# Kernel tuning notes

Hardware: AMD Instinct MI355X
Metric: run time of the kernel (lower is better)

Reference implementation:

```python
import jax, jax.numpy as jnp
import numpy as np

# SLAYER neuron / simulation constants (from params)
THETA = 10.0      # spike threshold
TAU_SR = 10.0     # PSP (synaptic response) time constant
TS = 1.0          # simulation time step
TAU_RHO = 1.0     # surrogate-gradient width
SCALE_RHO = 1.0   # surrogate-gradient scale
ALPHA = float(np.exp(-TS / TAU_SR))  # leaky-filter decay per step

B, C_IN, T = 32, 156, 2048
HID, OUT = 512, 20


@jax.custom_vjp
def spike(u):
    # Hard threshold with SLAYER-style exponential surrogate gradient.
    return (u >= THETA).astype(u.dtype)

def _spike_fwd(u):
    return spike(u), u

def _spike_bwd(u, g):
    sg = (SCALE_RHO / TAU_RHO) * jnp.exp(-jnp.abs(u - THETA) / TAU_RHO)
    return (g * sg,)

spike.defvjp(_spike_fwd, _spike_bwd)


def psp(x):
    # Leaky exponential temporal filter along the LAST axis (SLAYER psp):
    # y[t] = ALPHA * y[t-1] + x[t]
    xt = jnp.moveaxis(x, -1, 0)  # [T, ...]
    def step(c, xi):
        c = ALPHA * c + xi
        return c, c
    _, y = jax.lax.scan(step, jnp.zeros_like(xt[0]), xt)
    return jnp.moveaxis(y, 0, -1)


def dense(x, W):
    # SLAYER dense layer: per-timestep fully-connected over channel dim.
    # x: [N, C, H, W, T], W: [O, C] -> [N, O, H, W, T]
    return jnp.einsum('oc,nchwt->nohwt', W, x)


def _make_perm():
    rng = np.random.default_rng(0)
    random_list = rng.permutation(np.arange(1, 40))
    perm = []
    for i in random_list:
        perm.append(2 * int(i) - 2)
        perm.append(2 * int(i) - 1)
    for i in random_list:
        perm.append(2 * int(i) - 2 + 78)
        perm.append(2 * int(i) - 1 + 78)
    return jnp.asarray(perm, dtype=jnp.int32)


def setup_inputs() -> dict:
    key = jax.random.key(0)
    k0, k1, k2, k3, k4 = jax.random.split(key, 5)
    spike_input = jax.random.randint(k0, (B, C_IN, 1, 1, T), 0, 2).astype(jnp.float32)
    W1 = jax.random.normal(k1, (HID, C_IN), dtype=jnp.float32) * (C_IN ** -0.5)
    W2 = jax.random.normal(k2, (OUT, HID), dtype=jnp.float32) * (HID ** -0.5)
    Wl1 = jax.random.normal(k3, (HID, T), dtype=jnp.float32) * (T ** -0.5)
    Wl2 = jax.random.normal(k4, (OUT, HID), dtype=jnp.float32) * (HID ** -0.5)
    perm = _make_perm()
    return {"spike_input": spike_input, "W1": W1, "W2": W2,
            "Wl1": Wl1, "Wl2": Wl2, "perm": perm}


def reference(spike_input, W1, W2, Wl1, Wl2, perm):
    # Branch 1: channel-dense over taxels, PSP + spike, twice.
    s1 = spike(psp(dense(spike_input, W1)))          # [B, HID, 1, 1, T]
    spike_output = spike(psp(dense(s1, W2)))         # [B, OUT, 1, 1, T]

    # Branch 2: transpose channel<->time, permute taxel axis, dense over time dim.
    x_t = jnp.swapaxes(spike_input, 1, 4)            # [B, T, 1, 1, C_IN]
    x_tp = x_t[..., perm]                            # gather on taxel axis
    l1 = spike(psp(dense(x_tp, Wl1)))                # [B, HID, 1, 1, C_IN]
    location_output = spike(psp(dense(l1, Wl2)))     # [B, OUT, 1, 1, C_IN]

    return jnp.concatenate([spike_output, location_output], axis=4)
```

## Files before the change

### kernel.cpp

```cpp
#include <hip/hip_runtime.h>

#define ALPHA  0.90483741803595952f
#define ALPHA8 0.44932896411722156f
#define THETA  10.0f
#define BF1    ((unsigned short)0x3F80)
#define ISCALE 0.015625f

typedef short   bf16x8 __attribute__((ext_vector_type(8)));
typedef float   f32x4  __attribute__((ext_vector_type(4)));
typedef float   f32x4v __attribute__((ext_vector_type(4)));
typedef unsigned short ushort4v __attribute__((ext_vector_type(4)));
typedef unsigned short ushort8v __attribute__((ext_vector_type(8)));
typedef unsigned char  uchar4v  __attribute__((ext_vector_type(4)));
typedef unsigned char  uchar8v  __attribute__((ext_vector_type(8)));
typedef long long i64;

__device__ __forceinline__ unsigned short f2bf(float f) {
    unsigned int x = __float_as_uint(f);
    unsigned int r = (x + 0x7FFFu + ((x >> 16) & 1u)) >> 16;
    return (unsigned short)r;
}
__device__ __forceinline__ float bf2f(unsigned short h) {
    return __uint_as_float(((unsigned int)h) << 16);
}
__device__ __forceinline__ void split2(float w, unsigned short& h0,
                                       unsigned short& h1) {
    h0 = f2bf(w);          float r0 = w - bf2f(h0);
    h1 = f2bf(r0);
}
__device__ __forceinline__ unsigned char f2fp8(float f) {
    int pk = __builtin_amdgcn_cvt_pk_fp8_f32(f, 0.f, 0, false);
    return (unsigned char)(pk & 0xFF);
}
__device__ __forceinline__ float fp82f(unsigned char b) {
    return __builtin_amdgcn_cvt_f32_fp8((int)b, 0);
}

__global__ __launch_bounds__(256) void prep_scan_pack(
    const float* __restrict__ In, unsigned char* __restrict__ Infp8,
    unsigned short* __restrict__ Pbf,
    const float* __restrict__ W1,  const float* __restrict__ W2,
    const float* __restrict__ Wl1, const float* __restrict__ Wl2,
    unsigned short* __restrict__ W1p,  unsigned char* __restrict__ W2p8,
    unsigned char* __restrict__ Wl1p8, unsigned short* __restrict__ Wl2p)
{
    const int blk = blockIdx.x;
    if (blk >= 4992) {
        const int bidx = blk - 4992;
        if (bidx >= 512 && bidx < 544) {
            int m = bidx - 512;
            for (int k = threadIdx.x; k < 512; k += 256) {
                float w = (m < 20) ? W2[(long long)m * 512 + k] : 0.f;
                unsigned char h0 = f2fp8(w);
                unsigned char h1 = f2fp8(w - fp82f(h0));
                W2p8[(long long)m * 512 + k] = h0;
                W2p8[16384 + (long long)m * 512 + k] = h1;
            }
        } else if (bidx >= 544 && bidx < 1056) {
            int m = bidx - 544;
            for (int k = threadIdx.x; k < 2048; k += 256) {
                float w = Wl1[(long long)m * 2048 + k] * 64.0f;
                unsigned char h0 = f2fp8(w);
                unsigned char h1 = f2fp8(w - fp82f(h0));
                Wl1p8[(long long)m * 2048 + k] = h0;
                Wl1p8[1048576 + (long long)m * 2048 + k] = h1;
            }
        } else {
            const float* W; unsigned short* P; int M, K, Kp, Mp, m;
            if (bidx < 512) { W = W1;  P = W1p;  M = 512; K = 156; Kp = 160; Mp = 512; m = bidx; }
            else            { W = Wl2; P = Wl2p; M = 20;  K = 512; Kp = 512; Mp = 32;  m = bidx - 1056; }
            for (int k = threadIdx.x; k < Kp; k += 256) {
                float v = (m < M && k < K) ? W[(long long)m * K + k] : 0.f;
                unsigned short h0, h1;
                split2(v, h0, h1);
                P[(long long)m * Kp + k] = h0;
                P[(long long)Mp * Kp + (long long)m * Kp + k] = h1;
            }
        }
        return;
    }

    const int row = blk;
    const int tid = threadIdx.x;
    const float* x = In + (long long)row * 2048 + tid * 8;
    const unsigned char ONE8 = f2fp8(1.0f);

    float v[8];
    *(f32x4v*)&v[0] = *(const f32x4v*)x;
    *(f32x4v*)&v[4] = *(const f32x4v*)(x + 4);

    uchar8v raw;
    #pragma unroll
    for (int k = 0; k < 8; ++k) raw[k] = (v[k] >= 0.5f) ? ONE8 : (unsigned char)0;
    *(uchar8v*)(Infp8 + (long long)row * 2048 + tid * 8) = raw;

    float y = 0.f;
    #pragma unroll
    for (int k = 0; k < 8; ++k) { y = ALPHA * y + v[k]; v[k] = y; }

    __shared__ float sc[256];
    float val = y;
    sc[tid] = val;
    float m = ALPHA8;
    for (int d = 1; d < 256; d <<= 1) {
        __syncthreads();
        float p = (tid >= d) ? sc[tid - d] : 0.f;
        __syncthreads();
        val += m * p;
        sc[tid] = val;
        m *= m;
    }
    __syncthreads();
    float carry = (tid > 0) ? sc[tid - 1] : 0.f;

    ushort8v pv;
    float ak = ALPHA;
    #pragma unroll
    for (int k = 0; k < 8; ++k) {
        float yk = v[k] + ak * carry;
        ak *= ALPHA;
        pv[k] = f2bf(yk);
    }
    *(ushort8v*)(Pbf + (long long)row * 2048 + tid * 8) = pv;
}

__global__ __launch_bounds__(256) void transposeP(
    const unsigned short* __restrict__ Pbf, unsigned short* __restrict__ PT)
{
    __shared__ unsigned short Tile[64][72];
    const int t0 = blockIdx.x * 64;
    const int c0 = blockIdx.y * 64;
    const int b  = blockIdx.z;
    const int tid = threadIdx.x;

    #pragma unroll
    for (int s = 0; s < 2; ++s) {
        int id = tid + s * 256;
        int cc = id >> 3;
        int t8 = (id & 7) * 8;
        ushort8v v = {0,0,0,0,0,0,0,0};
        if (c0 + cc < 156)
            v = *(const ushort8v*)(Pbf + (long long)(b * 156 + c0 + cc) * 2048 + t0 + t8);
        *(ushort8v*)&Tile[cc][t8] = v;
    }
    __syncthreads();

    #pragma unroll
    for (int s = 0; s < 2; ++s) {
        int id = tid + s * 256;
        int t  = id >> 3;
        int c8 = (id & 7) * 8;
        if (c0 + c8 + 7 < 160) {
            unsigned short r[8];
            #pragma unroll
            for (int j = 0; j < 8; ++j) r[j] = Tile[c8 + j][t];
            *(ushort8v*)(PT + (long long)b * 327680 + (long long)(t0 + t) * 160 + c0 + c8)
                = *(ushort8v*)r;
        }
    }
}

__global__ __launch_bounds__(256) void mega_gemm1(
    const unsigned short* __restrict__ W1p,
    const unsigned short* __restrict__ PT,
    unsigned short* __restrict__ S1bits,
    const unsigned char* __restrict__ Wl1p8,
    const unsigned char* __restrict__ Infp8,
    unsigned short* __restrict__ Zp)
{
    __shared__ alignas(16) unsigned char SMEM[30720];
    const int bx  = blockIdx.x;
    const int tid = threadIdx.x;
    const int lane = tid & 63, w = tid >> 6;
    const int wy = w >> 1, wx = w & 1;
    const int l15 = lane & 15, kq = lane >> 4;

    if (bx < 2048) {
        auto As = (unsigned short (*)[128][40])SMEM;
        auto Bs = (unsigned short (*)[40])(SMEM + 20480);

        const int z  = bx >> 6;
        const int m0 = ((bx >> 4) & 3) * 128;
        const int n0 = (bx & 15) * 128;
        const unsigned short* Tb = PT + (long long)z * 327680;

        int aPl[4], aM[4], aK8[4];
        #pragma unroll
        for (int s = 0; s < 4; ++s) {
            int id = tid + s * 256;
            aPl[s] = id >> 9; int rem = id & 511;
            aM[s] = rem >> 2; aK8[s] = (rem & 3) * 8;
        }
        int bT[2], bC8[2];
        #pragma unroll
        for (int s = 0; s < 2; ++s) {
            int id = tid + s * 256;
            bT[s] = id >> 2; bC8[s] = (id & 3) * 8;
        }

        f32x4 acc[4][4] = {};
        ushort8v aReg[4], bReg[2];

        #pragma unroll
        for (int s = 0; s < 4; ++s)
            aReg[s] = *(const ushort8v*)(W1p + (long long)aPl[s] * 81920 +
                                         (long long)(m0 + aM[s]) * 160 + aK8[s]);
        #pragma unroll
        for (int s = 0; s < 2; ++s)
            bReg[s] = *(const ushort8v*)(Tb + (long long)(n0 + bT[s]) * 160 + bC8[s]);
        #pragma unroll
        for (int s = 0; s < 4; ++s) *(ushort8v*)&As[aPl[s]][aM[s]][aK8[s]] = aReg[s];
        #pragma unroll
        for (int s = 0; s < 2; ++s) *(ushort8v*)&Bs[bT[s]][bC8[s]] = bReg[s];
        __syncthreads();

        #pragma unroll
        for (int it = 0; it < 5; ++it) {
            const int kn = (it + 1) * 32;
            if (it < 4) {
                #pragma unroll
                for (int s = 0; s < 4; ++s)
                    aReg[s] = *(const ushort8v*)(W1p + (long long)aPl[s] * 81920 +
                                                 (long long)(m0 + aM[s]) * 160 + kn + aK8[s]);
                #pragma unroll
                for (int s = 0; s < 2; ++s)
                    bReg[s] = *(const ushort8v*)(Tb + (long long)(n0 + bT[s]) * 160 + kn + bC8[s]);
            }

            bf16x8 bfr[4];
            #pragma unroll
            for (int nt = 0; nt < 4; ++nt)
                bfr[nt] = *(const bf16x8*)&Bs[wx * 64 + nt * 16 + l15][kq * 8];
            #pragma unroll
            for (int s = 0; s < 2; ++s) {
                #pragma unroll
                for (int mt = 0; mt < 4; ++mt) {
                    bf16x8 afr = *(const bf16x8*)&As[s][wy * 64 + mt * 16 + l15][kq * 8];
                    #pragma unroll
                    for (int nt = 0; nt < 4; ++nt)
                        acc[mt][nt] = __builtin_amdgcn_mfma_f32_16x16x32_bf16(
                            afr, bfr[nt], acc[mt][nt], 0, 0, 0);
                }
            }
            __syncthreads();
            if (it < 4) {
                #pragma unroll
                for (int s = 0; s < 4; ++s) *(ushort8v*)&As[aPl[s]][aM[s]][aK8[s]] = aReg[s];
                #pragma unroll
                for (int s = 0; s < 2; ++s) *(ushort8v*)&Bs[bT[s]][bC8[s]] = bReg[s];
                __syncthreads();
            }
        }

        unsigned short* Db = S1bits + (long long)z * 512 * 128;
        #pragma unroll
        for (int mt = 0; mt < 4; ++mt) {
            #pragma unroll
            for (int i = 0; i < 4; ++i) {
                int m = m0 + wy * 64 + mt * 16 + kq * 4 + i;
                #pragma unroll
                for (int nt = 0; nt < 4; ++nt) {
                    unsigned long long mask = __ballot(acc[mt][nt][i] >= THETA);
                    if (l15 == 0) {
                        int nchunk = (n0 + wx * 64 + nt * 16) >> 4;
                        Db[(long long)m * 128 + nchunk] =
                            (unsigned short)((mask >> (kq * 16)) & 0xFFFFu);
                    }
                }
            }
        }
    } else {
        auto As8 = (unsigned char (*)[64][72])SMEM;
        auto Bs8 = (unsigned char (*)[72])(SMEM + 9216);

        const int id0 = bx - 2048;
        const int nIdx = id0 % 40;
        if (nIdx >= 39) return;
        const int rest = id0 / 40;
        const int n0  = nIdx * 128;
        const int m0  = (rest & 7) * 64;
        const int ksl = rest >> 3;
        const int ks0 = ksl * 512;

        int aPl[4], aM[4], aK8[4];
        #pragma unroll
        for (int s = 0; s < 4; ++s) {
            int id = tid + s * 256;
            aPl[s] = id >> 9; int rem = id & 511;
            aM[s] = rem >> 3; aK8[s] = (rem & 7) * 8;
        }
        int bN[4], bK8[4];
        #pragma unroll
        for (int s = 0; s < 4; ++s) {
            int id = tid + s * 256;
            bN[s] = id >> 3; bK8[s] = (id & 7) * 8;
        }

        f32x4 acc[2][4] = {};
        uchar8v aReg[4], bReg[4];

        #pragma unroll
        for (int s = 0; s < 4; ++s)
            aReg[s] = *(const uchar8v*)(Wl1p8 + (long long)aPl[s] * 1048576 +
                                        (long long)(m0 + aM[s]) * 2048 + ks0 + aK8[s]);
        #pragma unroll
        for (int s = 0; s < 4; ++s)
            bReg[s] = *(const uchar8v*)(Infp8 + (long long)(n0 + bN[s]) * 2048 + ks0 + bK8[s]);
        #pragma unroll
        for (int s = 0; s < 4; ++s) *(uchar8v*)&As8[aPl[s]][aM[s]][aK8[s]] = aReg[s];
        #pragma unroll
        for (int s = 0; s < 4; ++s) *(uchar8v*)&Bs8[bN[s]][bK8[s]] = bReg[s];
        __syncthreads();

        for (int it = 0; it < 8; ++it) {
            const int kn = ks0 + (it + 1) * 64;
            if (it < 7) {
                #pragma unroll
                for (int s = 0; s < 4; ++s)
                    aReg[s] = *(const uchar8v*)(Wl1p8 + (long long)aPl[s] * 1048576 +
                                                (long long)(m0 + aM[s]) * 2048 + kn + aK8[s]);
                #pragma unroll
                for (int s = 0; s < 4; ++s)
                    bReg[s] = *(const uchar8v*)(Infp8 + (long long)(n0 + bN[s]) * 2048 + kn + bK8[s]);
            }

            #pragma unroll
            for (int ks = 0; ks < 2; ++ks) {
                i64 bfr[4];
                #pragma unroll
                for (int nt = 0; nt < 4; ++nt)
                    bfr[nt] = *(const i64*)&Bs8[wx * 64 + nt * 16 + l15][ks * 32 + kq * 8];
                #pragma unroll
                for (int s = 0; s < 2; ++s) {
                    #pragma unroll
                    for (int mt = 0; mt < 2; ++mt) {
                        i64 afr = *(const i64*)&As8[s][wy * 32 + mt * 16 + l15][ks * 32 + kq * 8];
                        #pragma unroll
                        for (int nt = 0; nt < 4; ++nt)
                            acc[mt][nt] = __builtin_amdgcn_mfma_f32_16x16x32_fp8_fp8(
                                afr, bfr[nt], acc[mt][nt], 0, 0, 0);
                    }
                }
            }
            __syncthreads();
            if (it < 7) {
                #pragma unroll
                for (int s = 0; s < 4; ++s) *(uchar8v*)&As8[aPl[s]][aM[s]][aK8[s]] = aReg[s];
                #pragma unroll
                for (int s = 0; s < 4; ++s) *(uchar8v*)&Bs8[bN[s]][bK8[s]] = bReg[s];
                __syncthreads();
            }
        }

        unsigned short* Tu = (unsigned short*)SMEM;
        #pragma unroll
        for (int mt = 0; mt < 2; ++mt) {
            #pragma unroll
            for (int i = 0; i < 4; ++i) {
                int mL = wy * 32 + mt * 16 + kq * 4 + i;
                #pragma unroll
                for (int nt = 0; nt < 4; ++nt) {
                    int nL = wx * 64 + nt * 16 + l15;
                    Tu[mL * 129 + nL] = f2bf(acc[mt][nt][i] * ISCALE);
                }
            }
        }
        __syncthreads();

        unsigned short* Zs = Zp + (long long)ksl * 2555904;
        #pragma unroll
        for (int s2 = 0; s2 < 32; ++s2) {
            int id = tid + s2 * 256;
            int cL = id >> 6;
            int mL = id & 63;
            int n = n0 + cL;
            int bb = n / 156, cc = n - bb * 156;
            Zs[(long long)cc * 16384 + bb * 512 + m0 + mL] = Tu[mL * 129 + cL];
        }
    }
}

__global__ __launch_bounds__(256) void mega_stage2(
    const unsigned char* __restrict__ W2p8,
    const unsigned short* __restrict__ S1bits,
    float* __restrict__ C2p,
    const unsigned short* __restrict__ Zp,
    const int* __restrict__ perm,
    unsigned short* __restrict__ L1T)
{
    __shared__ alignas(16) unsigned char SMEM[20608];
    const int bx  = blockIdx.x;
    const int tid = threadIdx.x;

    if (bx < 1024) {
        auto As = (unsigned char (*)[32][72])SMEM;
        auto Bs = (unsigned char (*)[72])(SMEM + 4608);

        const int lane = tid & 63, w = tid >> 6;
        const int l15 = lane & 15, kq = lane >> 4;
        const int n0  = (bx & 15) * 128;
        const int ksl = (bx >> 4) & 1;
        const int b   = bx >> 5;
        const int ks0 = ksl * 256;

        const unsigned short* Bb = S1bits + (long long)b * 512 * 128;
        const unsigned char ONE8 = f2fp8(1.0f);

        int aPl[2], aM[2], aK8[2];
        #pragma unroll
        for (int s = 0; s < 2; ++s) {
            int id = tid + s * 256;
            aPl[s] = id >> 8; int rem = id & 255;
            aM[s] = rem >> 3; aK8[s] = (rem & 7) * 8;
        }
        const int kb = (tid >> 4) * 4;
        const int nb = (tid & 15) * 8;
        const int nchunk = (n0 + nb) >> 4;
        const int nshift = nb & 15;

        f32x4 acc[2][2] = {};
        uchar8v aReg[2];
        unsigned short bBits[4];

        auto loadA = [&](int k0) {
            #pragma unroll
            for (int s = 0; s < 2; ++s)
                aReg[s] = *(const uchar8v*)(W2p8 + (long long)aPl[s] * 16384 +
                                            (long long)aM[s] * 512 + k0 + aK8[s]);
        };
        auto loadB = [&](int k0) {
            #pragma unroll
            for (int kk2 = 0; kk2 < 4; ++kk2)
                bBits[kk2] = Bb[(long long)(k0 + kb + kk2) * 128 + nchunk];
        };
        auto stage = [&]() {
            #pragma unroll
            for (int s = 0; s < 2; ++s) *(uchar8v*)&As[aPl[s]][aM[s]][aK8[s]] = aReg[s];
            unsigned char bv[4][8];
            #pragma unroll
            for (int kk2 = 0; kk2 < 4; ++kk2) {
                unsigned int bits = ((unsigned int)bBits[kk2] >> nshift) & 0xFFu;
                #pragma unroll
                for (int j = 0; j < 8; ++j)
                    bv[kk2][j] = ((bits >> j) & 1u) ? ONE8 : (unsigned char)0;
            }
            #pragma unroll
            for (int j = 0; j < 8; ++j) {
                uchar4v v4 = { bv[0][j], bv[1][j], bv[2][j], bv[3][j] };
                *(uchar4v*)&Bs[nb + j][kb] = v4;
            }
        };

        loadA(ks0); loadB(ks0);
        stage();
        __syncthreads();

        #pragma unroll
        for (int it = 0; it < 4; ++it) {
            const int kn = ks0 + (it + 1) * 64;
            if (it < 3) { loadA(kn); loadB(kn); }

            #pragma unroll
            for (int ks = 0; ks < 2; ++ks) {
                i64 bfr[2];
                #pragma unroll
                for (int nt = 0; nt < 2; ++nt)
                    bfr[nt] = *(const i64*)&Bs[w * 32 + nt * 16 + l15][ks * 32 + kq * 8];
                #pragma unroll
                for (int s = 0; s < 2; ++s) {
                    #pragma unroll
                    for (int mt = 0; mt < 2; ++mt) {
                        i64 afr = *(const i64*)&As[s][mt * 16 + l15][ks * 32 + kq * 8];
                        #pragma unroll
                        for (int nt = 0; nt < 2; ++nt)
                            acc[mt][nt] = __builtin_amdgcn_mfma_f32_16x16x32_fp8_fp8(
                                afr, bfr[nt], acc[mt][nt], 0, 0, 0);
                    }
                }
            }
            __syncthreads();
            if (it < 3) {
                stage();
                __syncthreads();
            }
        }

        float* Cb = C2p + (long long)b * 20 * 2048 + (long long)ksl * 1310720LL;
        #pragma unroll
        for (int mt = 0; mt < 2; ++mt) {
            #pragma unroll
            for (int i = 0; i < 4; ++i) {
                int m = mt * 16 + kq * 4 + i;
                if (m >= 20) continue;
                #pragma unroll
                for (int nt = 0; nt < 2; ++nt) {
                    int n = n0 + w * 32 + nt * 16 + l15;
                    Cb[(long long)m * 2048 + n] = acc[mt][nt][i];
                }
            }
        }
    } else {
        auto Xs = (float (*)[32])SMEM;
        int* p  = (int*)(SMEM + 19968);

        const int r0 = (bx - 1024) * 32;
        for (int i = tid; i < 156; i += 256) p[i] = perm[i];

        const int row = tid & 31;
        const int cq  = tid >> 5;
        #pragma unroll
        for (int it = 0; it < 20; ++it) {
            int c = it * 8 + cq;
            if (c < 156) {
                long long base = (long long)c * 16384 + r0 + row;
                float s = bf2f(Zp[base]) + bf2f(Zp[base + 2555904]) +
                          bf2f(Zp[base + 2 * 2555904]) + bf2f(Zp[base + 3 * 2555904]);
                Xs[c][row] = s;
            }
        }
        __syncthreads();

        if (tid < 32) {
            float y = 0.f;
            for (int c = 0; c < 156; ++c) {
                y = ALPHA * y + Xs[p[c]][tid];
                L1T[(long long)c * 16384 + r0 + tid] = (y >= THETA) ? BF1 : 0;
            }
        }
    }
}

__global__ __launch_bounds__(256) void mega_stage3(
    const float* __restrict__ C2p, float* __restrict__ out,
    const unsigned short* __restrict__ Wl2p,
    const unsigned short* __restrict__ L1T,
    float* __restrict__ Cl2)
{
    __shared__ alignas(16) unsigned char SMEM[27648];
    const int bx  = blockIdx.x;
    const int tid = threadIdx.x;

    if (bx < 640) {
        float* sc = (float*)SMEM;
        const int row = bx;
        const float* x = C2p + (long long)row * 2048 + tid * 8;

        float v[8];
        #pragma unroll
        for (int k = 0; k < 8; ++k) v[k] = x[k] + x[k + 1310720LL];

        float y = 0.f;
        #pragma unroll
        for (int k = 0; k < 8; ++k) { y = ALPHA * y + v[k]; v[k] = y; }

        float val = y;
        sc[tid] = val;
        float m = ALPHA8;
        for (int d = 1; d < 256; d <<= 1) {
            __syncthreads();
            float p = (tid >= d) ? sc[tid - d] : 0.f;
            __syncthreads();
            val += m * p;
            sc[tid] = val;
            m *= m;
        }
        __syncthreads();
        float carry = (tid > 0) ? sc[tid - 1] : 0.f;

        float* o = out + (long long)row * 2204 + tid * 8;
        float ak = ALPHA;
        #pragma unroll
        for (int k = 0; k < 8; ++k) {
            float yk = v[k] + ak * carry;
            ak *= ALPHA;
            o[k] = (yk >= THETA) ? 1.0f : 0.0f;
        }
    } else {
        auto As = (unsigned short (*)[32][72])SMEM;
        auto Bs = (unsigned short (*)[72])(SMEM + 9216);

        const int id2 = bx - 640;
        const int n0 = (id2 & 1) * 128;
        const int b  = id2 >> 1;
        const int lane = tid & 63, w = tid >> 6;
        const int l15 = lane & 15, kq = lane >> 4;

        f32x4 acc[2][2] = {};

        for (int k0 = 0; k0 < 512; k0 += 64) {
            #pragma unroll
            for (int s = 0; s < 2; ++s) {
                int id = tid + s * 256;
                int pl = id >> 8, rem = id & 255;
                int m = rem >> 3, k8 = (rem & 7) * 8;
                ushort8v v = *(const ushort8v*)(Wl2p + (long long)pl * 16384 +
                                                (long long)m * 512 + k0 + k8);
                *(ushort8v*)&As[pl][m][k8] = v;
            }
            #pragma unroll
            for (int s = 0; s < 4; ++s) {
                int id = tid + s * 256;
                int n = id >> 3, k8 = (id & 7) * 8;
                ushort8v v = {0,0,0,0,0,0,0,0};
                if (n0 + n < 156)
                    v = *(const ushort8v*)(L1T + (long long)(n0 + n) * 16384 +
                                           b * 512 + k0 + k8);
                *(ushort8v*)&Bs[n][k8] = v;
            }
            __syncthreads();

            #pragma unroll
            for (int ks = 0; ks < 2; ++ks) {
                bf16x8 bfr[2];
                #pragma unroll
                for (int nt = 0; nt < 2; ++nt)
                    bfr[nt] = *(const bf16x8*)&Bs[w * 32 + nt * 16 + l15][ks * 32 + kq * 8];
                #pragma unroll
                for (int s = 0; s < 2; ++s) {
                    #pragma unroll
                    for (int mt = 0; mt < 2; ++mt) {
                        bf16x8 afr = *(const bf16x8*)&As[s][mt * 16 + l15][ks * 32 + kq * 8];
                        #pragma unroll
                        for (int nt = 0; nt < 2; ++nt)
                            acc[mt][nt] = __builtin_amdgcn_mfma_f32_16x16x32_bf16(
                                afr, bfr[nt], acc[mt][nt], 0, 0, 0);
                    }
                }
            }
            __syncthreads();
        }

        float* Cb = Cl2 + (long long)b * 20 * 156;
        #pragma unroll
        for (int mt = 0; mt < 2; ++mt) {
            #pragma unroll
            for (int i = 0; i < 4; ++i) {
                int m = mt * 16 + kq * 4 + i;
                if (m >= 20) continue;
                #pragma unroll
                for (int nt = 0; nt < 2; ++nt) {
                    int n = n0 + w * 32 + nt * 16 + l15;
                    if (n < 156) Cb[(long long)m * 156 + n] = acc[mt][nt][i];
                }
            }
        }
    }
}

__global__ __launch_bounds__(256) void scan_spike_C_out(
    const float* __restrict__ in, float* __restrict__ out, int rows)
{
    int row = blockIdx.x * blockDim.x + threadIdx.x;
    if (row >= rows) return;
    const float* x = in + (long long)row * 156;
    float* o = out + (long long)row * 2204 + 2048;
    float y = 0.f;
    for (int c = 0; c < 156; ++c) {
        y = ALPHA * y + x[c];
        o[c] = (y >= THETA) ? 1.0f : 0.0f;
    }
}

extern "C" void kernel_launch(void* const* d_in, const int* in_sizes, int n_in,
                              void* d_out, int out_size, void* d_ws, size_t ws_size,
                              hipStream_t stream)
{
    const float* In  = (const float*)d_in[0];
    const float* W1  = (const float*)d_in[1];
    const float* W2  = (const float*)d_in[2];
    const float* Wl1 = (const float*)d_in[3];
    const float* Wl2 = (const float*)d_in[4];
    const int*  perm = (const int*)d_in[5];
    float* out = (float*)d_out;

    float* ws = (float*)d_ws;
    unsigned short* S1bits = (unsigned short*)ws;
    float* C2p = ws + 1048576LL;
    unsigned char*  Infp8 = (unsigned char*)(ws + 3670016LL);
    unsigned short* Pbf  = (unsigned short*)(ws + 6225920LL);
    unsigned short* PT   = (unsigned short*)(ws + 11337728LL);
    unsigned short* W1p  = (unsigned short*)(ws + 16580608LL);
    unsigned char*  W2p8 = (unsigned char*)(ws + 16662528LL);
    unsigned char*  Wl1p8= (unsigned char*)(ws + 16670720LL);
    unsigned short* Wl2p = (unsigned short*)(ws + 17195008LL);
    unsigned short* Zpbf = (unsigned short*)(ws + 17211392LL);
    unsigned short* L1T  = (unsigned short*)(ws + 22323200LL);
    float* Cl2 = ws + 23601152LL;

    dim3 blk(256);

    prep_scan_pack<<<dim3(6080), blk, 0, stream>>>(
        In, Infp8, Pbf, W1, W2, Wl1, Wl2, W1p, W2p8, Wl1p8, Wl2p);
    transposeP<<<dim3(32, 3, 32), blk, 0, stream>>>(Pbf, PT);

    mega_gemm1<<<dim3(3328), blk, 0, stream>>>(W1p, PT, S1bits,
                                               Wl1p8, Infp8, Zpbf);
    mega_stage2<<<dim3(1536), blk, 0, stream>>>(W2p8, S1bits, C2p,
                                                Zpbf, perm, L1T);
    mega_stage3<<<dim3(704), blk, 0, stream>>>(C2p, out, Wl2p, L1T, Cl2);
    scan_spike_C_out<<<dim3(3), blk, 0, stream>>>(Cl2, out, 640);

    (void)in_sizes; (void)n_in; (void)out_size; (void)ws_size;
}
```

Baseline: 206.3 us.

## Fuse PSP scan with transpose into prep kernel using warp-shuffle scan

Removes the separate transposeP kernel and the intermediate Pbf buffer. The prep kernel now handles 8 channel rows per block: each thread scans 64 timesteps serially, a 32-lane shuffle scan with ALPHA^64 carries state across lanes, and the bf16 results are staged in shared memory and written straight out in the time-major [t][160] layout. This saves a full global write and re-read of the PSP tensor plus one kernel launch. The cost is much higher register use (64-float arrays), fewer blocks, a long serial dependence chain per thread, and strided 16-byte stores with a 320-byte stride.

```diff
diff --git a/kernel.cpp b/kernel.cpp
--- a/kernel.cpp
+++ b/kernel.cpp
@@ -1,10 +1,11 @@
 #include <hip/hip_runtime.h>
 
 #define ALPHA  0.90483741803595952f
-#define ALPHA8 0.44932896411722156f
+#define ALPHA64 0.0016615572731739337f
 #define THETA  10.0f
 #define BF1    ((unsigned short)0x3F80)
 #define ISCALE 0.015625f
+#define ALPHA8  0.44932896411722156f
 
 typedef short   bf16x8 __attribute__((ext_vector_type(8)));
 typedef float   f32x4  __attribute__((ext_vector_type(4)));
@@ -38,15 +39,15 @@
 
 __global__ __launch_bounds__(256) void prep_scan_pack(
     const float* __restrict__ In, unsigned char* __restrict__ Infp8,
-    unsigned short* __restrict__ Pbf,
+    unsigned short* __restrict__ PT,
     const float* __restrict__ W1,  const float* __restrict__ W2,
     const float* __restrict__ Wl1, const float* __restrict__ Wl2,
     unsigned short* __restrict__ W1p,  unsigned char* __restrict__ W2p8,
     unsigned char* __restrict__ Wl1p8, unsigned short* __restrict__ Wl2p)
 {
     const int blk = blockIdx.x;
-    if (blk >= 4992) {
-        const int bidx = blk - 4992;
+    if (blk >= 640) {
+        const int bidx = blk - 640;
         if (bidx >= 512 && bidx < 544) {
             int m = bidx - 512;
             for (int k = threadIdx.x; k < 512; k += 256) {
@@ -80,83 +81,70 @@
         return;
     }
 
-    const int row = blk;
+    __shared__ unsigned short Pt[8][2056];
+    const int b  = blk / 20;
+    const int g  = blk % 20;
+    const int c0 = g * 8;
+    const int nRows = (c0 + 8 <= 156) ? 8 : (156 - c0);
+
     const int tid = threadIdx.x;
-    const float* x = In + (long long)row * 2048 + tid * 8;
+    const int g8  = tid >> 5;
+    const int l   = tid & 31;
+    const bool live = (g8 < nRows);
     const unsigned char ONE8 = f2fp8(1.0f);
 
-    float v[8];
-    *(f32x4v*)&v[0] = *(const f32x4v*)x;
-    *(f32x4v*)&v[4] = *(const f32x4v*)(x + 4);
-
-    uchar8v raw;
-    #pragma unroll
-    for (int k = 0; k < 8; ++k) raw[k] = (v[k] >= 0.5f) ? ONE8 : (unsigned char)0;
-    *(uchar8v*)(Infp8 + (long long)row * 2048 + tid * 8) = raw;
-
-    float y = 0.f;
-    #pragma unroll
-    for (int k = 0; k < 8; ++k) { y = ALPHA * y + v[k]; v[k] = y; }
-
-    __shared__ float sc[256];
-    float val = y;
-    sc[tid] = val;
-    float m = ALPHA8;
-    for (int d = 1; d < 256; d <<= 1) {
-        __syncthreads();
-        float p = (tid >= d) ? sc[tid - d] : 0.f;
-        __syncthreads();
-        val += m * p;
-        sc[tid] = val;
-        m *= m;
+    float v[64];
+    if (live) {
+        const int row = b * 156 + c0 + g8;
+        const float* x = In + (long long)row * 2048 + l * 64;
+        #pragma unroll
+        for (int q = 0; q < 16; ++q)
+            *(f32x4v*)&v[q * 4] = *(const f32x4v*)(x + q * 4);
+
+        unsigned char raw[64];
+        #pragma unroll
+        for (int k = 0; k < 64; ++k)
+            raw[k] = (v[k] >= 0.5f) ? ONE8 : (unsigned char)0;
+        unsigned char* dst = Infp8 + (long long)row * 2048 + l * 64;
+        #pragma unroll
+        for (int q = 0; q < 8; ++q)
+            *(uchar8v*)(dst + q * 8) = *(uchar8v*)&raw[q * 8];
+
+        float y = 0.f;
+        #pragma unroll
+        for (int k = 0; k < 64; ++k) { y = ALPHA * y + v[k]; v[k] = y; }
+
+        float val = y;
+        float m = ALPHA64;
+        #pragma unroll
+        for (int d = 1; d < 32; d <<= 1) {
+            float p = __shfl_up(val, d, 32);
+            if (l >= d) val += m * p;
+            m *= m;
+        }
+        float carry = __shfl_up(val, 1, 32);
+        if (l == 0) carry = 0.f;
+
+        float ak = ALPHA;
+        #pragma unroll
+        for (int k = 0; k < 64; ++k) {
+            float yk = v[k] + ak * carry;
+            ak *= ALPHA;
+            Pt[g8][l * 64 + k] = f2bf(yk);
+        }
+    } else {
+        for (int k = l; k < 2048; k += 32) Pt[g8][k] = 0;
     }
     __syncthreads();
-    float carry = (tid > 0) ? sc[tid - 1] : 0.f;
-
-    ushort8v pv;
-    float ak = ALPHA;
+
+    unsigned short* Pb = PT + (long long)b * 327680 + c0;
     #pragma unroll
-    for (int k = 0; k < 8; ++k) {
-        float yk = v[k] + ak * carry;
-        ak *= ALPHA;
-        pv[k] = f2bf(yk);
-    }
-    *(ushort8v*)(Pbf + (long long)row * 2048 + tid * 8) = pv;
-}
-
-__global__ __launch_bounds__(256) void transposeP(
-    const unsigned short* __restrict__ Pbf, unsigned short* __restrict__ PT)
-{
-    __shared__ unsigned short Tile[64][72];
-    const int t0 = blockIdx.x * 64;
-    const int c0 = blockIdx.y * 64;
-    const int b  = blockIdx.z;
-    const int tid = threadIdx.x;
-
-    #pragma unroll
-    for (int s = 0; s < 2; ++s) {
-        int id = tid + s * 256;
-        int cc = id >> 3;
-        int t8 = (id & 7) * 8;
-        ushort8v v = {0,0,0,0,0,0,0,0};
-        if (c0 + cc < 156)
-            v = *(const ushort8v*)(Pbf + (long long)(b * 156 + c0 + cc) * 2048 + t0 + t8);
-        *(ushort8v*)&Tile[cc][t8] = v;
-    }
-    __syncthreads();
-
-    #pragma unroll
-    for (int s = 0; s < 2; ++s) {
-        int id = tid + s * 256;
-        int t  = id >> 3;
-        int c8 = (id & 7) * 8;
-        if (c0 + c8 + 7 < 160) {
-            unsigned short r[8];
-            #pragma unroll
-            for (int j = 0; j < 8; ++j) r[j] = Tile[c8 + j][t];
-            *(ushort8v*)(PT + (long long)b * 327680 + (long long)(t0 + t) * 160 + c0 + c8)
-                = *(ushort8v*)r;
-        }
+    for (int it = 0; it < 8; ++it) {
+        int t = tid + it * 256;
+        unsigned short r[8];
+        #pragma unroll
+        for (int c = 0; c < 8; ++c) r[c] = Pt[c][t];
+        *(ushort8v*)(Pb + (long long)t * 160) = *(ushort8v*)r;
     }
 }
 
@@ -677,7 +665,6 @@
     unsigned short* S1bits = (unsigned short*)ws;
     float* C2p = ws + 1048576LL;
     unsigned char*  Infp8 = (unsigned char*)(ws + 3670016LL);
-    unsigned short* Pbf  = (unsigned short*)(ws + 6225920LL);
     unsigned short* PT   = (unsigned short*)(ws + 11337728LL);
     unsigned short* W1p  = (unsigned short*)(ws + 16580608LL);
     unsigned char*  W2p8 = (unsigned char*)(ws + 16662528LL);
@@ -689,9 +676,8 @@
 
     dim3 blk(256);
 
-    prep_scan_pack<<<dim3(6080), blk, 0, stream>>>(
-        In, Infp8, Pbf, W1, W2, Wl1, Wl2, W1p, W2p8, Wl1p8, Wl2p);
-    transposeP<<<dim3(32, 3, 32), blk, 0, stream>>>(Pbf, PT);
+    prep_scan_pack<<<dim3(1728), blk, 0, stream>>>(
+        In, Infp8, PT, W1, W2, Wl1, Wl2, W1p, W2p8, Wl1p8, Wl2p);
 
     mega_gemm1<<<dim3(3328), blk, 0, stream>>>(W1p, PT, S1bits,
                                                Wl1p8, Infp8, Zpbf);
```

New measurement: 215.4 us. 4.4% more time.
